# Performance work log

Hardware: AMD Instinct MI355X
Metric: run time of the kernel (lower is better)

Reference implementation:

```python
import jax, jax.numpy as jnp
import numpy as np
from jax import lax

STRIDE0, WS, PS, K = 4, 9, 3, 10
LVLS = 4
_MEAN = jnp.array([0.485, 0.456, 0.406], jnp.float32).reshape(1, 1, 3, 1, 1)
_STD = jnp.array([0.229, 0.224, 0.225], jnp.float32).reshape(1, 1, 3, 1, 1)


def _conv7(x, w, b):
    y = lax.conv_general_dilated(x, w, (1, 1), ((3, 3), (3, 3)),
                                 dimension_numbers=('NCHW', 'OIHW', 'NCHW'))
    return y + b[None, :, None, None]


def _basic(x, l, Ws):
    w1, b1, w2, b2, w3, b3, w4, b4, w5, b5 = [W[l] for W in Ws]
    x = jax.nn.relu(_conv7(x, w1, b1))
    x = jax.nn.relu(_conv7(x, w2, b2))
    x = jax.nn.relu(_conv7(x, w3, b3))
    x = jax.nn.relu(_conv7(x, w4, b4))
    return _conv7(x, w5, b5)


def _pool2(x):
    N, C, H, W = x.shape
    return x.reshape(N, C, H // 2, 2, W // 2, 2).mean(axis=(3, 5))


def _bsample(img, y, x):
    # img [N,C,H,W]; y,x [N,Hq,Wq] absolute float coords; border-clamped bilinear
    N, C, H, W = img.shape
    y = jnp.clip(y, 0., H - 1.)
    x = jnp.clip(x, 0., W - 1.)
    y0 = jnp.floor(y)
    x0 = jnp.floor(x)
    wy = (y - y0)[:, None]
    wx = (x - x0)[:, None]
    y0i = y0.astype(jnp.int32)
    x0i = x0.astype(jnp.int32)
    y1i = jnp.minimum(y0i + 1, H - 1)
    x1i = jnp.minimum(x0i + 1, W - 1)
    imgf = img.reshape(N, C, H * W)

    def g(yi, xi):
        idx = (yi * W + xi).reshape(N, 1, -1)
        return jnp.take_along_axis(imgf, idx, 2).reshape(N, C, *y.shape[1:])

    return (g(y0i, x0i) * (1 - wy) * (1 - wx) + g(y0i, x1i) * (1 - wy) * wx
            + g(y1i, x0i) * wy * (1 - wx) + g(y1i, x1i) * wy * wx)


def _spynet(ref, supp, Ws):
    # coarse-to-fine residual flow estimation (SpyNet)
    refs, sups = [ref], [supp]
    for _ in range(LVLS - 1):
        refs.append(_pool2(refs[-1]))
        sups.append(_pool2(sups[-1]))
    N = ref.shape[0]
    Hc, Wc = refs[-1].shape[2:]
    flow = jnp.zeros((N, 2, Hc, Wc), ref.dtype)
    for l in range(LVLS - 1, -1, -1):
        Hl, Wl = refs[l].shape[2:]
        if l < LVLS - 1:
            flow = 2. * jax.image.resize(flow, (N, 2, Hl, Wl), 'bilinear')
        gy, gx = jnp.meshgrid(jnp.arange(Hl, dtype=flow.dtype),
                              jnp.arange(Wl, dtype=flow.dtype), indexing='ij')
        warped = _bsample(sups[l], gy[None] + flow[:, 1], gx[None] + flow[:, 0])
        flow = flow + _basic(jnp.concatenate([refs[l], warped, flow], 1), l, Ws)
    return flow


def _bgather(vidf, ry, rx, H, W, C):
    # vidf [B,T,C,H*W]; ry,rx [B,T,*rest] float coords pre-clipped to valid range
    B, T = vidf.shape[:2]
    rest = ry.shape[2:]
    y0 = jnp.floor(ry)
    x0 = jnp.floor(rx)
    wy = (ry - y0)[:, :, None]
    wx = (rx - x0)[:, :, None]
    y0i = y0.astype(jnp.int32)
    x0i = x0.astype(jnp.int32)
    y1i = jnp.minimum(y0i + 1, H - 1)
    x1i = jnp.minimum(x0i + 1, W - 1)

    def g(yi, xi):
        idx = (yi * W + xi).reshape(B, T, 1, -1)
        return jnp.take_along_axis(vidf, idx, 3).reshape(B, T, C, *rest)

    return (g(y0i, x0i) * (1 - wy) * (1 - wx) + g(y0i, x1i) * (1 - wy) * wx
            + g(y1i, x0i) * wy * (1 - wx) + g(y1i, x1i) * wy * wx)


def _forward(vid, Ws):
    B, T, C, H, W = vid.shape
    # --- SpyNet flows between consecutive frames ---
    nv = (vid - _MEAN) / _STD
    ref = nv[:, :-1].reshape(B * (T - 1), C, H, W)
    sup = nv[:, 1:].reshape(B * (T - 1), C, H, W)
    fflow = _spynet(ref, sup, Ws).reshape(B, T - 1, 2, H, W)
    bflow = _spynet(sup, ref, Ws).reshape(B, T - 1, 2, H, W)
    z = jnp.zeros((B, 1, 2, H, W), vid.dtype)
    fflow = jnp.concatenate([fflow, z], 1)  # flow t -> t+1 (last frame zero)
    bflow = jnp.concatenate([z, bflow], 1)  # flow t -> t-1 (first frame zero)

    # --- flow-guided windowed non-local search (wt=1, skip_self=False) ---
    nH, nW = H // STRIDE0, W // STRIDE0
    qh = jnp.arange(nH) * STRIDE0
    qw = jnp.arange(nW) * STRIDE0
    fg = fflow[:, :, :, qh][:, :, :, :, qw]  # [B,T,2,nH,nW] flow at query grid
    bg = bflow[:, :, :, qh][:, :, :, :, qw]
    dp = jnp.arange(PS) - PS // 2
    offs = jnp.arange(WS) - WS // 2
    oh = jnp.repeat(offs, WS).astype(vid.dtype)  # [WS*WS] row offsets
    ow = jnp.tile(offs, WS).astype(vid.dtype)    # [WS*WS] col offsets

    # query patches (integer grid, clamped)
    yqi = jnp.clip(qh[:, None] + dp[None], 0, H - 1)
    xqi = jnp.clip(qw[:, None] + dp[None], 0, W - 1)
    qp = vid[:, :, :, yqi][..., xqi]           # [B,T,C,nH,PS,nW,PS]
    qp = qp.transpose(0, 1, 2, 3, 5, 4, 6)     # [B,T,C,nH,nW,PS,PS]
    qpe = qp[:, :, :, :, :, None, None]        # broadcast over (ws,ws)

    vidf = vid.reshape(B, T, C, H * W)
    qhf = qh.astype(vid.dtype)
    qwf = qw.astype(vid.dtype)
    offsf = offs.astype(vid.dtype)
    dpf = dp.astype(vid.dtype)
    zf = jnp.zeros((B, T, nH, nW), vid.dtype)

    flows_k = []
    for dt, fh, fw in ((0, zf, zf), (1, fg[:, :, 1], fg[:, :, 0]),
                       (-1, bg[:, :, 1], bg[:, :, 0])):
        tid = jnp.clip(jnp.arange(T) + dt, 0, T - 1)
        frf = vidf[:, tid]  # target frames, edge-clamped in time
        ry = (qhf[None, None, :, None, None, None] + fh[:, :, :, :, None, None]
              + offsf[None, None, None, None, :, None]
              + dpf[None, None, None, None, None, :])  # [B,T,nH,nW,WS,PS]
        rx = (qwf[None, None, None, :, None, None] + fw[:, :, :, :, None, None]
              + offsf[None, None, None, None, :, None]
              + dpf[None, None, None, None, None, :])
        ry = jnp.clip(ry, 0., H - 1.)
        rx = jnp.clip(rx, 0., W - 1.)
        RY = jnp.broadcast_to(ry[:, :, :, :, :, None, :, None],
                              (B, T, nH, nW, WS, WS, PS, PS))
        RX = jnp.broadcast_to(rx[:, :, :, :, None, :, None, :],
                              (B, T, nH, nW, WS, WS, PS, PS))
        cand = _bgather(frf, RY, RX, H, W, C)  # [B,T,C,nH,nW,WS,WS,PS,PS]
        dist = ((qpe - cand) ** 2).sum(axis=(2, -2, -1))  # [B,T,nH,nW,WS,WS]
        dist = dist.reshape(B, T, nH, nW, WS * WS)
        _, idx = lax.top_k(-dist, K)  # [B,T,nH,nW,K]
        dh = fh[..., None] + oh[idx]
        dw = fw[..., None] + ow[idx]
        dts = jnp.full_like(dh, float(dt))
        flows_k.append(jnp.stack([dts, dh, dw], axis=-1))
    return jnp.concatenate(flows_k, axis=-2)  # [B,T,nH,nW,3*K,3]


def setup_inputs():
    key = jax.random.key(0)
    ks = jax.random.split(key, 6)
    B, T, C, H, W = 1, 4, 3, 192, 192
    L = LVLS

    def w(k, shape):
        return jax.random.normal(k, shape, jnp.float32) * 0.02

    return {
        "vid": jax.random.normal(ks[0], (B, T, C, H, W), jnp.float32),
        "w1": w(ks[1], (L, 32, 8, 7, 7)), "b1": jnp.zeros((L, 32), jnp.float32),
        "w2": w(ks[2], (L, 64, 32, 7, 7)), "b2": jnp.zeros((L, 64), jnp.float32),
        "w3": w(ks[3], (L, 32, 64, 7, 7)), "b3": jnp.zeros((L, 32), jnp.float32),
        "w4": w(ks[4], (L, 16, 32, 7, 7)), "b4": jnp.zeros((L, 16), jnp.float32),
        "w5": w(ks[5], (L, 2, 16, 7, 7)), "b5": jnp.zeros((L, 2), jnp.float32),
    }


def reference(vid, w1, b1, w2, b2, w3, b3, w4, b4, w5, b5):
    return _forward(vid, (w1, b1, w2, b2, w3, b3, w4, b4, w5, b5))
```

## Files before the change

### kernel.cpp

```cpp
#include <hip/hip_runtime.h>
#include <cstdint>

#define H0 192
#define W0 192
#define TT 4
#define NBATCH 6

__global__ void k_normalize(const float* __restrict__ vid, float* __restrict__ nv) {
    int idx = blockIdx.x * 256 + threadIdx.x;
    const int total = TT * 3 * H0 * W0;
    if (idx >= total) return;
    int c = (idx / (H0 * W0)) % 3;
    float m = (c == 0) ? 0.485f : (c == 1) ? 0.456f : 0.406f;
    float s = (c == 0) ? 0.229f : (c == 1) ? 0.224f : 0.225f;
    nv[idx] = (vid[idx] - m) / s;
}

__global__ void k_pool(const float* __restrict__ in, float* __restrict__ out,
                       int NC, int Ho, int Wo) {
    int idx = blockIdx.x * 256 + threadIdx.x;
    int total = NC * Ho * Wo;
    if (idx >= total) return;
    int x = idx % Wo;
    int y = (idx / Wo) % Ho;
    int nc = idx / (Wo * Ho);
    const float* p = in + ((size_t)nc * (Ho * 2) + y * 2) * (size_t)(Wo * 2) + x * 2;
    int Wi = Wo * 2;
    out[idx] = (p[0] + p[1] + p[Wi] + p[Wi + 1]) * 0.25f;
}

__global__ void k_upsample2x(const float* __restrict__ in, float* __restrict__ out,
                             int NC, int Hi, int Wi) {
    int Ho = Hi * 2, Wo = Wi * 2;
    int idx = blockIdx.x * 256 + threadIdx.x;
    int total = NC * Ho * Wo;
    if (idx >= total) return;
    int x = idx % Wo;
    int y = (idx / Wo) % Ho;
    int nc = idx / (Wo * Ho);
    int ky = y >> 1, kx = x >> 1;
    int y0, y1, x0, x1;
    float wy0, wy1, wx0, wx1;
    if ((y & 1) == 0) {
        if (ky == 0) { y0 = 0; y1 = 0; wy0 = 1.f; wy1 = 0.f; }
        else { y0 = ky - 1; y1 = ky; wy0 = 0.25f; wy1 = 0.75f; }
    } else {
        if (ky == Hi - 1) { y0 = ky; y1 = ky; wy0 = 1.f; wy1 = 0.f; }
        else { y0 = ky; y1 = ky + 1; wy0 = 0.75f; wy1 = 0.25f; }
    }
    if ((x & 1) == 0) {
        if (kx == 0) { x0 = 0; x1 = 0; wx0 = 1.f; wx1 = 0.f; }
        else { x0 = kx - 1; x1 = kx; wx0 = 0.25f; wx1 = 0.75f; }
    } else {
        if (kx == Wi - 1) { x0 = kx; x1 = kx; wx0 = 1.f; wx1 = 0.f; }
        else { x0 = kx; x1 = kx + 1; wx0 = 0.75f; wx1 = 0.25f; }
    }
    const float* base = in + (size_t)nc * Hi * Wi;
    float v = wy0 * (wx0 * base[(size_t)y0 * Wi + x0] + wx1 * base[(size_t)y0 * Wi + x1])
            + wy1 * (wx0 * base[(size_t)y1 * Wi + x0] + wx1 * base[(size_t)y1 * Wi + x1]);
    out[idx] = 2.0f * v;
}

__global__ void k_build_in8(const float* __restrict__ pyr, const float* __restrict__ flow,
                            float* __restrict__ in8, int H, int W) {
    int idx = blockIdx.x * 256 + threadIdx.x;
    int total = NBATCH * H * W;
    if (idx >= total) return;
    int x = idx % W;
    int y = (idx / W) % H;
    int n = idx / (W * H);
    int ref_f = (n < 3) ? n : n - 2;
    int sup_f = (n < 3) ? n + 1 : n - 3;
    size_t hw = (size_t)H * W;
    float fx = flow[((size_t)n * 2 + 0) * hw + (size_t)y * W + x];
    float fy = flow[((size_t)n * 2 + 1) * hw + (size_t)y * W + x];
    float ry = (float)y + fy;
    float rx = (float)x + fx;
    ry = fminf(fmaxf(ry, 0.f), (float)(H - 1));
    rx = fminf(fmaxf(rx, 0.f), (float)(W - 1));
    float y0f = floorf(ry), x0f = floorf(rx);
    float wy = ry - y0f, wx = rx - x0f;
    int y0 = (int)y0f, x0 = (int)x0f;
    int y1 = min(y0 + 1, H - 1), x1 = min(x0 + 1, W - 1);
    const float* sup = pyr + (size_t)sup_f * 3 * hw;
    const float* ref = pyr + (size_t)ref_f * 3 * hw;
    float* o = in8 + (size_t)n * 8 * hw + (size_t)y * W + x;
    #pragma unroll
    for (int c = 0; c < 3; c++) {
        const float* sc = sup + (size_t)c * hw;
        float g00 = sc[(size_t)y0 * W + x0], g01 = sc[(size_t)y0 * W + x1];
        float g10 = sc[(size_t)y1 * W + x0], g11 = sc[(size_t)y1 * W + x1];
        float v = g00 * (1.f - wy) * (1.f - wx) + g01 * (1.f - wy) * wx
                + g10 * wy * (1.f - wx) + g11 * wy * wx;
        o[(size_t)(3 + c) * hw] = v;
        o[(size_t)c * hw] = ref[(size_t)c * hw + (size_t)y * W + x];
    }
    o[6 * hw] = fx;
    o[7 * hw] = fy;
}

#define BSH 38
#define BSTR 39
#define BSZ (BSH * BSTR)
template<int OCB, bool RELU, bool ACC>
__global__ __launch_bounds__(256) void k_conv_big(
        const float* __restrict__ in, const float* __restrict__ wt,
        const float* __restrict__ bias, float* __restrict__ out,
        int IC, int OC, int H, int W, int nt, int nocg) {
    __shared__ float sm[2 * BSZ];
    int nwg = gridDim.x;
    int wg = blockIdx.x;
    int q = nwg >> 3, r = nwg & 7;
    int xcd = wg & 7, pos = wg >> 3;
    int logical = ((xcd < r) ? xcd * (q + 1) : r * (q + 1) + (xcd - r) * q) + pos;
    int ocg = logical % nocg; int t2 = logical / nocg;
    int tx = t2 % nt; t2 /= nt;
    int ty = t2 % nt; int n = t2 / nt;
    int oc0 = ocg * OCB;
    int bx = tx * 32, by = ty * 32;
    int tid = threadIdx.x;
    int tq = tid & 7, trow = tid >> 3;
    int hw = H * W;

    int saddr[6]; int goff[6]; bool gval[6];
    #pragma unroll
    for (int k = 0; k < 6; k++) {
        int tpos = tid + k * 256;
        int ly = tpos / BSH, lx = tpos - ly * BSH;
        int gy = by + ly - 3, gx = bx + lx - 3;
        bool tv = tpos < BSH * BSH;
        bool v = tv && ((unsigned)gy < (unsigned)H) && ((unsigned)gx < (unsigned)W);
        saddr[k] = tv ? ly * BSTR + lx : (BSZ - 1);
        goff[k] = v ? gy * W + gx : 0;
        gval[k] = v;
    }

    float acc[OCB][4];
    #pragma unroll
    for (int o = 0; o < OCB; o++)
        #pragma unroll
        for (int p = 0; p < 4; p++) acc[o][p] = 0.f;

    const float* ip0 = in + (size_t)n * IC * hw;
    float sreg[6];
    #pragma unroll
    for (int k = 0; k < 6; k++) sreg[k] = gval[k] ? ip0[goff[k]] : 0.f;
    #pragma unroll
    for (int k = 0; k < 6; k++) sm[saddr[k]] = sreg[k];
    if (IC > 1) {
        const float* ip1 = ip0 + hw;
        #pragma unroll
        for (int k = 0; k < 6; k++) sreg[k] = gval[k] ? ip1[goff[k]] : 0.f;
    }
    __syncthreads();

    int tof = trow * BSTR + tq * 4;
    for (int ic = 0; ic < IC; ++ic) {
        int cur = ic & 1;
        if (ic + 1 < IC) {
            float* dst = sm + (cur ^ 1) * BSZ;
            #pragma unroll
            for (int k = 0; k < 6; k++) dst[saddr[k]] = sreg[k];
            if (ic + 2 < IC) {
                const float* ip = ip0 + (size_t)(ic + 2) * hw;
                #pragma unroll
                for (int k = 0; k < 6; k++) sreg[k] = gval[k] ? ip[goff[k]] : 0.f;
            }
        }
        const float* smc = sm + cur * BSZ + tof;
        const float* wic = wt + (size_t)ic * 49;
        #pragma unroll
        for (int ky = 0; ky < 7; ++ky) {
            float xin[10];
            #pragma unroll
            for (int off = 0; off < 10; off++) xin[off] = smc[ky * BSTR + off];
            #pragma unroll
            for (int oc = 0; oc < OCB; ++oc) {
                const float* wr = wic + (size_t)(oc0 + oc) * IC * 49 + ky * 7;
                #pragma unroll
                for (int kx = 0; kx < 7; ++kx) {
                    float wv = wr[kx];
                    #pragma unroll
                    for (int p = 0; p < 4; p++)
                        acc[oc][p] = fmaf(xin[kx + p], wv, acc[oc][p]);
                }
            }
        }
        __syncthreads();
    }

    int oy = by + trow, ox0 = bx + tq * 4;
    if (oy < H) {
        #pragma unroll
        for (int oc = 0; oc < OCB; ++oc) {
            float bv = bias[oc0 + oc];
            float v[4];
            #pragma unroll
            for (int p = 0; p < 4; p++) {
                v[p] = acc[oc][p] + bv;
                if (RELU) v[p] = fmaxf(v[p], 0.f);
            }
            float* op = out + ((size_t)n * OC + oc0 + oc) * hw + (size_t)oy * W + ox0;
            if (ox0 + 3 < W) {
                if (ACC) {
                    float4 o4 = *(const float4*)op;
                    o4.x += v[0]; o4.y += v[1]; o4.z += v[2]; o4.w += v[3];
                    *(float4*)op = o4;
                } else {
                    float4 o4 = make_float4(v[0], v[1], v[2], v[3]);
                    *(float4*)op = o4;
                }
            } else {
                #pragma unroll
                for (int p = 0; p < 4; p++)
                    if (ox0 + p < W) { if (ACC) op[p] += v[p]; else op[p] = v[p]; }
            }
        }
    }
}

#define SSH 22
#define SSTR 48
#define SSZ (SSH * SSTR)
template<int OCB, bool RELU, bool ACC>
__global__ __launch_bounds__(256) void k_conv_small(
        const float* __restrict__ in, const float* __restrict__ wt,
        const float* __restrict__ bias, float* __restrict__ out,
        int IC, int OC, int H, int W, int nocg) {
    __shared__ float sm[2 * SSZ];
    int tid = threadIdx.x;
    int tx = tid & 15, ty = tid >> 4;
    int bx = blockIdx.x * 16, by = blockIdx.y * 16;
    int ocg = blockIdx.z % nocg;
    int n = blockIdx.z / nocg;
    int oc0 = ocg * OCB;
    int hw = H * W;

    int saddr[2]; int goff[2]; bool gval[2];
    #pragma unroll
    for (int k = 0; k < 2; k++) {
        int tpos = tid + k * 256;
        int ly = tpos / SSH, lx = tpos - ly * SSH;
        int gy = by + ly - 3, gx = bx + lx - 3;
        bool tv = tpos < SSH * SSH;
        bool v = tv && ((unsigned)gy < (unsigned)H) && ((unsigned)gx < (unsigned)W);
        saddr[k] = tv ? ly * SSTR + lx : (SSZ - 1);
        goff[k] = v ? gy * W + gx : 0;
        gval[k] = v;
    }

    float acc[OCB];
    #pragma unroll
    for (int o = 0; o < OCB; o++) acc[o] = 0.f;

    const float* ip0 = in + (size_t)n * IC * hw;
    float sreg[2];
    #pragma unroll
    for (int k = 0; k < 2; k++) sreg[k] = gval[k] ? ip0[goff[k]] : 0.f;
    #pragma unroll
    for (int k = 0; k < 2; k++) sm[saddr[k]] = sreg[k];
    if (IC > 1) {
        const float* ip1 = ip0 + hw;
        #pragma unroll
        for (int k = 0; k < 2; k++) sreg[k] = gval[k] ? ip1[goff[k]] : 0.f;
    }
    __syncthreads();

    int tof = ty * SSTR + tx;
    for (int ic = 0; ic < IC; ++ic) {
        int cur = ic & 1;
        if (ic + 1 < IC) {
            float* dst = sm + (cur ^ 1) * SSZ;
            #pragma unroll
            for (int k = 0; k < 2; k++) dst[saddr[k]] = sreg[k];
            if (ic + 2 < IC) {
                const float* ip = ip0 + (size_t)(ic + 2) * hw;
                #pragma unroll
                for (int k = 0; k < 2; k++) sreg[k] = gval[k] ? ip[goff[k]] : 0.f;
            }
        }
        const float* smc = sm + cur * SSZ + tof;
        const float* wic = wt + (size_t)ic * 49;
        #pragma unroll
        for (int ky = 0; ky < 7; ++ky) {
            float xin[7];
            #pragma unroll
            for (int kx = 0; kx < 7; kx++) xin[kx] = smc[ky * SSTR + kx];
            #pragma unroll
            for (int oc = 0; oc < OCB; ++oc) {
                const float* wr = wic + (size_t)(oc0 + oc) * IC * 49 + ky * 7;
                #pragma unroll
                for (int kx = 0; kx < 7; ++kx)
                    acc[oc] = fmaf(xin[kx], wr[kx], acc[oc]);
            }
        }
        __syncthreads();
    }

    int oy = by + ty, ox = bx + tx;
    if (oy < H && ox < W) {
        #pragma unroll
        for (int oc = 0; oc < OCB; ++oc) {
            float v = acc[oc] + bias[oc0 + oc];
            if (RELU) v = fmaxf(v, 0.f);
            float* op = out + ((size_t)n * OC + oc0 + oc) * hw + (size_t)oy * W + ox;
            if (ACC) *op += v; else *op = v;
        }
    }
}

__global__ __launch_bounds__(64) void k_match(
        const float* __restrict__ vid, const float* __restrict__ flow,
        float* __restrict__ out) {
    int q = blockIdx.x;
    int j = q % 48; q /= 48;
    int i = q % 48; q /= 48;
    int t = q % 4;
    int dtIdx = q / 4;
    int lane = threadIdx.x;

    float fh = 0.f, fw = 0.f, dtf = 0.f;
    int tid = t;
    if (dtIdx == 1) {
        if (t < 3) {
            size_t base = (((size_t)t * 2) * 192 + i * 4) * 192 + j * 4;
            fw = flow[base];
            fh = flow[base + (size_t)192 * 192];
        }
        tid = min(t + 1, 3);
        dtf = 1.f;
    } else if (dtIdx == 2) {
        if (t > 0) {
            size_t base = (((size_t)(t + 2) * 2) * 192 + i * 4) * 192 + j * 4;
            fw = flow[base];
            fh = flow[base + (size_t)192 * 192];
        }
        tid = max(t - 1, 0);
        dtf = -1.f;
    }

    __shared__ int sy0[27], sy1[27], sx0[27], sx1[27];
    __shared__ float sfy[27], sfx[27], qp[27];
    if (lane < 27) {
        int wq = lane / 3, p = lane % 3;
        float ry = (((float)(i * 4) + fh) + (float)(wq - 4)) + (float)(p - 1);
        ry = fminf(fmaxf(ry, 0.f), 191.f);
        float y0f = floorf(ry);
        int y0 = (int)y0f;
        sy0[lane] = y0; sy1[lane] = min(y0 + 1, 191); sfy[lane] = ry - y0f;
        float rx = (((float)(j * 4) + fw) + (float)(wq - 4)) + (float)(p - 1);
        rx = fminf(fmaxf(rx, 0.f), 191.f);
        float x0f = floorf(rx);
        int x0 = (int)x0f;
        sx0[lane] = x0; sx1[lane] = min(x0 + 1, 191); sfx[lane] = rx - x0f;
        int c = lane / 9, pp = lane % 9, py = pp / 3, px = pp % 3;
        int yy = min(max(i * 4 + py - 1, 0), 191);
        int xx = min(max(j * 4 + px - 1, 0), 191);
        qp[lane] = vid[(((size_t)t * 3 + c) * 192 + yy) * 192 + xx];
    }
    __syncthreads();

    const float* frame = vid + (size_t)tid * 3 * 192 * 192;
    float dist[2];
    int widx[2];
    #pragma unroll
    for (int r = 0; r < 2; r++) {
        int w = lane + 64 * r;
        if (w < 81) {
            int wy = w / 9, wx = w % 9;
            float dsum = 0.f;
            for (int c = 0; c < 3; c++) {
                const float* fc = frame + (size_t)c * 36864;
                #pragma unroll
                for (int py = 0; py < 3; py++) {
                    int ye = wy * 3 + py;
                    int y0 = sy0[ye], y1 = sy1[ye];
                    float fy = sfy[ye];
                    const float* r0 = fc + (size_t)y0 * 192;
                    const float* r1 = fc + (size_t)y1 * 192;
                    #pragma unroll
                    for (int px = 0; px < 3; px++) {
                        int xe = wx * 3 + px;
                        int x0 = sx0[xe], x1 = sx1[xe];
                        float fx = sfx[xe];
                        float g00 = r0[x0], g01 = r0[x1], g10 = r1[x0], g11 = r1[x1];
                        float cand = g00 * (1.f - fy) * (1.f - fx) + g01 * (1.f - fy) * fx
                                   + g10 * fy * (1.f - fx) + g11 * fy * fx;
                        float diff = qp[(c * 3 + py) * 3 + px] - cand;
                        dsum = fmaf(diff, diff, dsum);
                    }
                }
            }
            dist[r] = dsum; widx[r] = w;
        } else {
            dist[r] = __builtin_inff(); widx[r] = 1000;
        }
    }

    for (int k = 0; k < 10; k++) {
        float d = dist[0]; int wi = widx[0];
        if (dist[1] < d || (dist[1] == d && widx[1] < wi)) { d = dist[1]; wi = widx[1]; }
        #pragma unroll
        for (int off = 32; off >= 1; off >>= 1) {
            float od = __shfl_xor(d, off);
            int ow = __shfl_xor(wi, off);
            if (od < d || (od == d && ow < wi)) { d = od; wi = ow; }
        }
        if (lane == 0) {
            size_t ob = ((((size_t)t * 48 + i) * 48 + j) * 30 + dtIdx * 10 + k) * 3;
            out[ob + 0] = dtf;
            out[ob + 1] = fh + (float)(wi / 9 - 4);
            out[ob + 2] = fw + (float)(wi % 9 - 4);
        }
        if (widx[0] == wi) dist[0] = __builtin_inff();
        if (widx[1] == wi) dist[1] = __builtin_inff();
    }
}

extern "C" void kernel_launch(void* const* d_in, const int* in_sizes, int n_in,
                              void* d_out, int out_size, void* d_ws, size_t ws_size,
                              hipStream_t stream) {
    const float* vid = (const float*)d_in[0];
    const float* w1 = (const float*)d_in[1];  const float* b1 = (const float*)d_in[2];
    const float* w2 = (const float*)d_in[3];  const float* b2 = (const float*)d_in[4];
    const float* w3 = (const float*)d_in[5];  const float* b3 = (const float*)d_in[6];
    const float* w4 = (const float*)d_in[7];  const float* b4 = (const float*)d_in[8];
    const float* w5 = (const float*)d_in[9];  const float* b5 = (const float*)d_in[10];
    float* out = (float*)d_out;
    float* ws = (float*)d_ws;

    float* nv    = ws;
    float* pyr1  = nv    + 442368;
    float* pyr2  = pyr1  + 110592;
    float* pyr3  = pyr2  + 27648;
    float* flowA = pyr3  + 6912;
    float* flowB = flowA + 442368;
    float* in8   = flowB + 442368;
    float* bufA  = in8   + 1769472;
    float* bufB  = bufA  + 7077888;

    k_normalize<<<(442368 + 255) / 256, 256, 0, stream>>>(vid, nv);
    k_pool<<<(110592 + 255) / 256, 256, 0, stream>>>(nv, pyr1, 12, 96, 96);
    k_pool<<<(27648 + 255) / 256, 256, 0, stream>>>(pyr1, pyr2, 12, 48, 48);
    k_pool<<<(6912 + 255) / 256, 256, 0, stream>>>(pyr2, pyr3, 12, 24, 24);

    const float* pyrs[4] = {nv, pyr1, pyr2, pyr3};

    float* cur = flowA;
    float* oth = flowB;
    hipMemsetAsync(cur, 0, (size_t)NBATCH * 2 * 24 * 24 * 4, stream);
    for (int l = 3; l >= 0; --l) {
        int H = H0 >> l, W = W0 >> l;
        if (l < 3) {
            k_upsample2x<<<((12 * H * W) + 255) / 256, 256, 0, stream>>>(cur, oth, 12, H / 2, W / 2);
            float* tsw = cur; cur = oth; oth = tsw;
        }
        k_build_in8<<<((NBATCH * H * W) + 255) / 256, 256, 0, stream>>>(pyrs[l], cur, in8, H, W);

        const float* W1 = w1 + (size_t)l * 32 * 8 * 49;  const float* B1 = b1 + l * 32;
        const float* W2 = w2 + (size_t)l * 64 * 32 * 49; const float* B2 = b2 + l * 64;
        const float* W3 = w3 + (size_t)l * 32 * 64 * 49; const float* B3 = b3 + l * 32;
        const float* W4 = w4 + (size_t)l * 16 * 32 * 49; const float* B4 = b4 + l * 16;
        const float* W5 = w5 + (size_t)l * 2 * 16 * 49;  const float* B5 = b5 + l * 2;

        if (l == 0) {
            int nt = 6;
            k_conv_big<8, true,  false><<<nt * nt * 4 * 6, 256, 0, stream>>>(in8,  W1, B1, bufA, 8,  32, H, W, nt, 4);
            k_conv_big<8, true,  false><<<nt * nt * 8 * 6, 256, 0, stream>>>(bufA, W2, B2, bufB, 32, 64, H, W, nt, 8);
            k_conv_big<8, true,  false><<<nt * nt * 4 * 6, 256, 0, stream>>>(bufB, W3, B3, bufA, 64, 32, H, W, nt, 4);
            k_conv_big<8, true,  false><<<nt * nt * 2 * 6, 256, 0, stream>>>(bufA, W4, B4, bufB, 32, 16, H, W, nt, 2);
            k_conv_big<2, false, true ><<<nt * nt * 1 * 6, 256, 0, stream>>>(bufB, W5, B5, cur,  16, 2,  H, W, nt, 1);
        } else {
            int t16 = (H + 15) / 16;
            k_conv_small<8, true,  false><<<dim3(t16, t16, 4 * 6), 256, 0, stream>>>(in8,  W1, B1, bufA, 8,  32, H, W, 4);
            k_conv_small<8, true,  false><<<dim3(t16, t16, 8 * 6), 256, 0, stream>>>(bufA, W2, B2, bufB, 32, 64, H, W, 8);
            k_conv_small<8, true,  false><<<dim3(t16, t16, 4 * 6), 256, 0, stream>>>(bufB, W3, B3, bufA, 64, 32, H, W, 4);
            k_conv_small<8, true,  false><<<dim3(t16, t16, 2 * 6), 256, 0, stream>>>(bufA, W4, B4, bufB, 32, 16, H, W, 2);
            k_conv_small<2, false, true ><<<dim3(t16, t16, 1 * 6), 256, 0, stream>>>(bufB, W5, B5, cur,  16, 2,  H, W, 1);
        }
    }

    k_match<<<27648, 64, 0, stream>>>(vid, cur, out);
}
```

Baseline: 3.755 ms.

## Unify conv kernels with LDS-staged weights and multi-row register tiles

```diff
diff --git a/kernel.cpp b/kernel.cpp
--- a/kernel.cpp
+++ b/kernel.cpp
@@ -99,212 +99,164 @@
     o[7 * hw] = fy;
 }
 
-#define BSH 38
-#define BSTR 39
-#define BSZ (BSH * BSTR)
-template<int OCB, bool RELU, bool ACC>
-__global__ __launch_bounds__(256) void k_conv_big(
+
+template<int NR, int ISZ>
+__device__ __forceinline__ void conv_iload(const float* __restrict__ ip, float* sreg,
+        int tid, int by, int bx, int H, int W) {
+    #pragma unroll
+    for (int k = 0; k < NR; k++) {
+        int tpos = tid + k * 256;
+        int ly = tpos / 39;
+        int lx = tpos - ly * 39;
+        int gy = by + ly - 3, gx = bx + lx - 3;
+        bool ok = (tpos < ISZ) && (lx < 38) && ((unsigned)gy < (unsigned)H) && ((unsigned)gx < (unsigned)W);
+        sreg[k] = ok ? ip[gy * W + gx] : 0.f;
+    }
+}
+
+template<int OCB, int NWR, int NWELEM>
+__device__ __forceinline__ void conv_wload(const float* __restrict__ wt, float* wreg,
+        int tid, int oc0, int IC, int cbase) {
+    #pragma unroll
+    for (int k = 0; k < NWR; k++) {
+        int tpos = tid + k * 256;
+        int oc = tpos / 392;
+        int rem = tpos - oc * 392;
+        int icc = rem / 49;
+        int kk = rem - icc * 49;
+        wreg[k] = (tpos < NWELEM) ? wt[((size_t)(oc0 + oc) * IC + (cbase + icc)) * 49 + kk] : 0.f;
+    }
+}
+
+template<int OCB, int RPT, bool RELU, bool ACC>
+__global__ __launch_bounds__(256) void k_conv(
         const float* __restrict__ in, const float* __restrict__ wt,
         const float* __restrict__ bias, float* __restrict__ out,
-        int IC, int OC, int H, int W, int nt, int nocg) {
-    __shared__ float sm[2 * BSZ];
-    int nwg = gridDim.x;
-    int wg = blockIdx.x;
+        int IC, int OC, int H, int W, int ntx, int nty, int nocg) {
+    constexpr int TH = RPT * 32;
+    constexpr int IROWS = TH + 6;
+    constexpr int ISZ = IROWS * 39;
+    constexpr int NR = (ISZ + 255) / 256;
+    constexpr int WROW = 52;
+    constexpr int NWELEM = OCB * 8 * 49;
+    constexpr int NWR = (NWELEM + 255) / 256;
+    __shared__ float smi[2 * ISZ];
+    __shared__ float smw[8 * OCB * WROW];
+
+    int nwg = gridDim.x, wg = blockIdx.x;
     int q = nwg >> 3, r = nwg & 7;
     int xcd = wg & 7, pos = wg >> 3;
     int logical = ((xcd < r) ? xcd * (q + 1) : r * (q + 1) + (xcd - r) * q) + pos;
     int ocg = logical % nocg; int t2 = logical / nocg;
-    int tx = t2 % nt; t2 /= nt;
-    int ty = t2 % nt; int n = t2 / nt;
+    int tx = t2 % ntx; t2 /= ntx;
+    int ty = t2 % nty; int n = t2 / nty;
     int oc0 = ocg * OCB;
-    int bx = tx * 32, by = ty * 32;
+    int bx = tx * 32, by = ty * TH;
     int tid = threadIdx.x;
     int tq = tid & 7, trow = tid >> 3;
     int hw = H * W;
 
-    int saddr[6]; int goff[6]; bool gval[6];
-    #pragma unroll
-    for (int k = 0; k < 6; k++) {
-        int tpos = tid + k * 256;
-        int ly = tpos / BSH, lx = tpos - ly * BSH;
-        int gy = by + ly - 3, gx = bx + lx - 3;
-        bool tv = tpos < BSH * BSH;
-        bool v = tv && ((unsigned)gy < (unsigned)H) && ((unsigned)gx < (unsigned)W);
-        saddr[k] = tv ? ly * BSTR + lx : (BSZ - 1);
-        goff[k] = v ? gy * W + gx : 0;
-        gval[k] = v;
-    }
-
-    float acc[OCB][4];
+    float acc[OCB][RPT][4];
     #pragma unroll
     for (int o = 0; o < OCB; o++)
         #pragma unroll
-        for (int p = 0; p < 4; p++) acc[o][p] = 0.f;
+        for (int rr = 0; rr < RPT; rr++)
+            #pragma unroll
+            for (int p = 0; p < 4; p++) acc[o][rr][p] = 0.f;
 
     const float* ip0 = in + (size_t)n * IC * hw;
-    float sreg[6];
-    #pragma unroll
-    for (int k = 0; k < 6; k++) sreg[k] = gval[k] ? ip0[goff[k]] : 0.f;
-    #pragma unroll
-    for (int k = 0; k < 6; k++) sm[saddr[k]] = sreg[k];
-    if (IC > 1) {
-        const float* ip1 = ip0 + hw;
-        #pragma unroll
-        for (int k = 0; k < 6; k++) sreg[k] = gval[k] ? ip1[goff[k]] : 0.f;
-    }
-    __syncthreads();
-
-    int tof = trow * BSTR + tq * 4;
+    float sreg[NR];
+    float wreg[NWR];
+
+    conv_wload<OCB, NWR, NWELEM>(wt, wreg, tid, oc0, IC, 0);
+    conv_iload<NR, ISZ>(ip0, sreg, tid, by, bx, H, W);
+    #pragma unroll
+    for (int k = 0; k < NR; k++) {
+        int tpos = tid + k * 256;
+        if (tpos < ISZ) smi[tpos] = sreg[k];
+    }
+    if (IC > 1) conv_iload<NR, ISZ>(ip0 + hw, sreg, tid, by, bx, H, W);
+
     for (int ic = 0; ic < IC; ++ic) {
         int cur = ic & 1;
+        if ((ic & 7) == 0) {
+            #pragma unroll
+            for (int k = 0; k < NWR; k++) {
+                int tpos = tid + k * 256;
+                int oc = tpos / 392;
+                int rem = tpos - oc * 392;
+                int icc = rem / 49;
+                int kk = rem - icc * 49;
+                if (tpos < NWELEM) smw[(icc * OCB + oc) * WROW + kk] = wreg[k];
+            }
+            __syncthreads();
+            if (ic + 8 < IC) conv_wload<OCB, NWR, NWELEM>(wt, wreg, tid, oc0, IC, ic + 8);
+        }
         if (ic + 1 < IC) {
-            float* dst = sm + (cur ^ 1) * BSZ;
-            #pragma unroll
-            for (int k = 0; k < 6; k++) dst[saddr[k]] = sreg[k];
-            if (ic + 2 < IC) {
-                const float* ip = ip0 + (size_t)(ic + 2) * hw;
-                #pragma unroll
-                for (int k = 0; k < 6; k++) sreg[k] = gval[k] ? ip[goff[k]] : 0.f;
+            #pragma unroll
+            for (int k = 0; k < NR; k++) {
+                int tpos = tid + k * 256;
+                if (tpos < ISZ) smi[(cur ^ 1) * ISZ + tpos] = sreg[k];
             }
-        }
-        const float* smc = sm + cur * BSZ + tof;
-        const float* wic = wt + (size_t)ic * 49;
+            if (ic + 2 < IC)
+                conv_iload<NR, ISZ>(ip0 + (size_t)(ic + 2) * hw, sreg, tid, by, bx, H, W);
+        }
+        int icc = ic & 7;
+        const float* smc = smi + cur * ISZ + trow * 39 + tq * 4;
         #pragma unroll
         for (int ky = 0; ky < 7; ++ky) {
-            float xin[10];
-            #pragma unroll
-            for (int off = 0; off < 10; off++) xin[off] = smc[ky * BSTR + off];
+            float xin[RPT][10];
+            #pragma unroll
+            for (int rr = 0; rr < RPT; rr++)
+                #pragma unroll
+                for (int off = 0; off < 10; off++)
+                    xin[rr][off] = smc[(rr * 32 + ky) * 39 + off];
             #pragma unroll
             for (int oc = 0; oc < OCB; ++oc) {
-                const float* wr = wic + (size_t)(oc0 + oc) * IC * 49 + ky * 7;
+                const float* wrow = smw + (icc * OCB + oc) * WROW + ky * 7;
                 #pragma unroll
                 for (int kx = 0; kx < 7; ++kx) {
-                    float wv = wr[kx];
+                    float wv = wrow[kx];
+                    #pragma unroll
+                    for (int rr = 0; rr < RPT; rr++)
+                        #pragma unroll
+                        for (int p = 0; p < 4; p++)
+                            acc[oc][rr][p] = fmaf(xin[rr][kx + p], wv, acc[oc][rr][p]);
+                }
+            }
+        }
+        __syncthreads();
+    }
+
+    int ox0 = bx + tq * 4;
+    #pragma unroll
+    for (int rr = 0; rr < RPT; rr++) {
+        int oy = by + trow + rr * 32;
+        if (oy < H) {
+            #pragma unroll
+            for (int oc = 0; oc < OCB; ++oc) {
+                float bv = bias[oc0 + oc];
+                float v[4];
+                #pragma unroll
+                for (int p = 0; p < 4; p++) {
+                    v[p] = acc[oc][rr][p] + bv;
+                    if (RELU) v[p] = fmaxf(v[p], 0.f);
+                }
+                float* op = out + ((size_t)n * OC + oc0 + oc) * hw + (size_t)oy * W + ox0;
+                if (ox0 + 3 < W) {
+                    if (ACC) {
+                        float4 o4 = *(const float4*)op;
+                        o4.x += v[0]; o4.y += v[1]; o4.z += v[2]; o4.w += v[3];
+                        *(float4*)op = o4;
+                    } else {
+                        *(float4*)op = make_float4(v[0], v[1], v[2], v[3]);
+                    }
+                } else {
                     #pragma unroll
                     for (int p = 0; p < 4; p++)
-                        acc[oc][p] = fmaf(xin[kx + p], wv, acc[oc][p]);
+                        if (ox0 + p < W) { if (ACC) op[p] += v[p]; else op[p] = v[p]; }
                 }
             }
-        }
-        __syncthreads();
-    }
-
-    int oy = by + trow, ox0 = bx + tq * 4;
-    if (oy < H) {
-        #pragma unroll
-        for (int oc = 0; oc < OCB; ++oc) {
-            float bv = bias[oc0 + oc];
-            float v[4];
-            #pragma unroll
-            for (int p = 0; p < 4; p++) {
-                v[p] = acc[oc][p] + bv;
-                if (RELU) v[p] = fmaxf(v[p], 0.f);
-            }
-            float* op = out + ((size_t)n * OC + oc0 + oc) * hw + (size_t)oy * W + ox0;
-            if (ox0 + 3 < W) {
-                if (ACC) {
-                    float4 o4 = *(const float4*)op;
-                    o4.x += v[0]; o4.y += v[1]; o4.z += v[2]; o4.w += v[3];
-                    *(float4*)op = o4;
-                } else {
-                    float4 o4 = make_float4(v[0], v[1], v[2], v[3]);
-                    *(float4*)op = o4;
-                }
-            } else {
-                #pragma unroll
-                for (int p = 0; p < 4; p++)
-                    if (ox0 + p < W) { if (ACC) op[p] += v[p]; else op[p] = v[p]; }
-            }
-        }
-    }
-}
-
-#define SSH 22
-#define SSTR 48
-#define SSZ (SSH * SSTR)
-template<int OCB, bool RELU, bool ACC>
-__global__ __launch_bounds__(256) void k_conv_small(
-        const float* __restrict__ in, const float* __restrict__ wt,
-        const float* __restrict__ bias, float* __restrict__ out,
-        int IC, int OC, int H, int W, int nocg) {
-    __shared__ float sm[2 * SSZ];
-    int tid = threadIdx.x;
-    int tx = tid & 15, ty = tid >> 4;
-    int bx = blockIdx.x * 16, by = blockIdx.y * 16;
-    int ocg = blockIdx.z % nocg;
-    int n = blockIdx.z / nocg;
-    int oc0 = ocg * OCB;
-    int hw = H * W;
-
-    int saddr[2]; int goff[2]; bool gval[2];
-    #pragma unroll
-    for (int k = 0; k < 2; k++) {
-        int tpos = tid + k * 256;
-        int ly = tpos / SSH, lx = tpos - ly * SSH;
-        int gy = by + ly - 3, gx = bx + lx - 3;
-        bool tv = tpos < SSH * SSH;
-        bool v = tv && ((unsigned)gy < (unsigned)H) && ((unsigned)gx < (unsigned)W);
-        saddr[k] = tv ? ly * SSTR + lx : (SSZ - 1);
-        goff[k] = v ? gy * W + gx : 0;
-        gval[k] = v;
-    }
-
-    float acc[OCB];
-    #pragma unroll
-    for (int o = 0; o < OCB; o++) acc[o] = 0.f;
-
-    const float* ip0 = in + (size_t)n * IC * hw;
-    float sreg[2];
-    #pragma unroll
-    for (int k = 0; k < 2; k++) sreg[k] = gval[k] ? ip0[goff[k]] : 0.f;
-    #pragma unroll
-    for (int k = 0; k < 2; k++) sm[saddr[k]] = sreg[k];
-    if (IC > 1) {
-        const float* ip1 = ip0 + hw;
-        #pragma unroll
-        for (int k = 0; k < 2; k++) sreg[k] = gval[k] ? ip1[goff[k]] : 0.f;
-    }
-    __syncthreads();
-
-    int tof = ty * SSTR + tx;
-    for (int ic = 0; ic < IC; ++ic) {
-        int cur = ic & 1;
-        if (ic + 1 < IC) {
-            float* dst = sm + (cur ^ 1) * SSZ;
-            #pragma unroll
-            for (int k = 0; k < 2; k++) dst[saddr[k]] = sreg[k];
-            if (ic + 2 < IC) {
-                const float* ip = ip0 + (size_t)(ic + 2) * hw;
-                #pragma unroll
-                for (int k = 0; k < 2; k++) sreg[k] = gval[k] ? ip[goff[k]] : 0.f;
-            }
-        }
-        const float* smc = sm + cur * SSZ + tof;
-        const float* wic = wt + (size_t)ic * 49;
-        #pragma unroll
-        for (int ky = 0; ky < 7; ++ky) {
-            float xin[7];
-            #pragma unroll
-            for (int kx = 0; kx < 7; kx++) xin[kx] = smc[ky * SSTR + kx];
-            #pragma unroll
-            for (int oc = 0; oc < OCB; ++oc) {
-                const float* wr = wic + (size_t)(oc0 + oc) * IC * 49 + ky * 7;
-                #pragma unroll
-                for (int kx = 0; kx < 7; ++kx)
-                    acc[oc] = fmaf(xin[kx], wr[kx], acc[oc]);
-            }
-        }
-        __syncthreads();
-    }
-
-    int oy = by + ty, ox = bx + tx;
-    if (oy < H && ox < W) {
-        #pragma unroll
-        for (int oc = 0; oc < OCB; ++oc) {
-            float v = acc[oc] + bias[oc0 + oc];
-            if (RELU) v = fmaxf(v, 0.f);
-            float* op = out + ((size_t)n * OC + oc0 + oc) * hw + (size_t)oy * W + ox;
-            if (ACC) *op += v; else *op = v;
         }
     }
 }
@@ -464,19 +416,18 @@
         const float* W5 = w5 + (size_t)l * 2 * 16 * 49;  const float* B5 = b5 + l * 2;
 
         if (l == 0) {
-            int nt = 6;
-            k_conv_big<8, true,  false><<<nt * nt * 4 * 6, 256, 0, stream>>>(in8,  W1, B1, bufA, 8,  32, H, W, nt, 4);
-            k_conv_big<8, true,  false><<<nt * nt * 8 * 6, 256, 0, stream>>>(bufA, W2, B2, bufB, 32, 64, H, W, nt, 8);
-            k_conv_big<8, true,  false><<<nt * nt * 4 * 6, 256, 0, stream>>>(bufB, W3, B3, bufA, 64, 32, H, W, nt, 4);
-            k_conv_big<8, true,  false><<<nt * nt * 2 * 6, 256, 0, stream>>>(bufA, W4, B4, bufB, 32, 16, H, W, nt, 2);
-            k_conv_big<2, false, true ><<<nt * nt * 1 * 6, 256, 0, stream>>>(bufB, W5, B5, cur,  16, 2,  H, W, nt, 1);
+            k_conv<4, 2, true,  false><<<6 * 3 * 8 * 6, 256, 0, stream>>>(in8,  W1, B1, bufA, 8,  32, H, W, 6, 3, 8);
+            k_conv<8, 2, true,  false><<<6 * 3 * 8 * 6, 256, 0, stream>>>(bufA, W2, B2, bufB, 32, 64, H, W, 6, 3, 8);
+            k_conv<4, 2, true,  false><<<6 * 3 * 8 * 6, 256, 0, stream>>>(bufB, W3, B3, bufA, 64, 32, H, W, 6, 3, 8);
+            k_conv<2, 2, true,  false><<<6 * 3 * 8 * 6, 256, 0, stream>>>(bufA, W4, B4, bufB, 32, 16, H, W, 6, 3, 8);
+            k_conv<1, 1, false, true ><<<6 * 6 * 2 * 6, 256, 0, stream>>>(bufB, W5, B5, cur,  16, 2,  H, W, 6, 6, 2);
         } else {
-            int t16 = (H + 15) / 16;
-            k_conv_small<8, true,  false><<<dim3(t16, t16, 4 * 6), 256, 0, stream>>>(in8,  W1, B1, bufA, 8,  32, H, W, 4);
-            k_conv_small<8, true,  false><<<dim3(t16, t16, 8 * 6), 256, 0, stream>>>(bufA, W2, B2, bufB, 32, 64, H, W, 8);
-            k_conv_small<8, true,  false><<<dim3(t16, t16, 4 * 6), 256, 0, stream>>>(bufB, W3, B3, bufA, 64, 32, H, W, 4);
-            k_conv_small<8, true,  false><<<dim3(t16, t16, 2 * 6), 256, 0, stream>>>(bufA, W4, B4, bufB, 32, 16, H, W, 2);
-            k_conv_small<2, false, true ><<<dim3(t16, t16, 1 * 6), 256, 0, stream>>>(bufB, W5, B5, cur,  16, 2,  H, W, 1);
+            int nt = (H + 31) / 32;
+            k_conv<4, 1, true,  false><<<nt * nt * 8 * 6, 256, 0, stream>>>(in8,  W1, B1, bufA, 8,  32, H, W, nt, nt, 8);
+            k_conv<8, 1, true,  false><<<nt * nt * 8 * 6, 256, 0, stream>>>(bufA, W2, B2, bufB, 32, 64, H, W, nt, nt, 8);
+            k_conv<4, 1, true,  false><<<nt * nt * 8 * 6, 256, 0, stream>>>(bufB, W3, B3, bufA, 64, 32, H, W, nt, nt, 8);
+            k_conv<2, 1, true,  false><<<nt * nt * 8 * 6, 256, 0, stream>>>(bufA, W4, B4, bufB, 32, 16, H, W, nt, nt, 8);
+            k_conv<1, 1, false, true ><<<nt * nt * 2 * 6, 256, 0, stream>>>(bufB, W5, B5, cur,  16, 2,  H, W, nt, nt, 2);
         }
     }
 
```

Result: faster. 3.472 ms (-7.5%).
